# Kernel optimization log

Hardware: AMD Instinct MI355X
Metric: run time of the kernel (lower is better)

## Reference

```python
import jax, jax.numpy as jnp
import numpy as np

B, S, H = 1, 4096, 2048
NH, NKV, HD = 16, 4, 128  # query heads, kv heads, head_dim
THETA = 1000000.0
NEG = -1e9


def setup_inputs() -> dict:
    key = jax.random.key(0)
    ks = jax.random.split(key, 5)
    hidden_states = jax.random.normal(ks[0], (B, S, H), jnp.float32) * 0.02
    Wq = jax.random.normal(ks[1], (H, NH * HD), jnp.float32) * 0.02
    Wk = jax.random.normal(ks[2], (H, NKV * HD), jnp.float32) * 0.02
    Wv = jax.random.normal(ks[3], (H, NKV * HD), jnp.float32) * 0.02
    Wo = jax.random.normal(ks[4], (H, H), jnp.float32) * 0.02
    # additive causal mask [B,1,S,S]
    causal = jnp.tril(jnp.ones((S, S), bool))
    attention_mask = jnp.where(causal, 0.0, NEG).astype(jnp.float32)[None, None]
    position_ids = jnp.arange(S, dtype=jnp.int32)[None]
    return dict(hidden_states=hidden_states, Wq=Wq, Wk=Wk, Wv=Wv, Wo=Wo,
                attention_mask=attention_mask, position_ids=position_ids)


def _rotate_half(x):
    return jnp.concatenate([-x[..., HD // 2:], x[..., :HD // 2]], axis=-1)


def reference(hidden_states, Wq, Wk, Wv, Wo, attention_mask, position_ids):
    # projections -> [B, heads, S, HD]
    q = (hidden_states @ Wq).reshape(B, S, NH, HD).transpose(0, 2, 1, 3)
    k = (hidden_states @ Wk).reshape(B, S, NKV, HD).transpose(0, 2, 1, 3)
    v = (hidden_states @ Wv).reshape(B, S, NKV, HD).transpose(0, 2, 1, 3)

    # RoPE (HF style: freqs duplicated across halves, rotate_half)
    inv_freq = 1.0 / (THETA ** (jnp.arange(0, HD, 2, dtype=jnp.float32) / HD))
    freqs = position_ids.astype(jnp.float32)[..., None] * inv_freq  # [B,S,HD/2]
    emb = jnp.concatenate([freqs, freqs], axis=-1)                  # [B,S,HD]
    cos = jnp.cos(emb)[:, None].astype(q.dtype)                     # [B,1,S,HD]
    sin = jnp.sin(emb)[:, None].astype(q.dtype)
    q = q * cos + _rotate_half(q) * sin
    k = k * cos + _rotate_half(k) * sin

    # GQA: repeat each kv head consecutively (matches torch repeat_kv)
    rep = NH // NKV
    k = jnp.repeat(k, rep, axis=1)
    v = jnp.repeat(v, rep, axis=1)

    scale = 1.0 / jnp.sqrt(jnp.float32(HD))
    scores = jnp.einsum('bhqd,bhkd->bhqk', q, k) * scale + attention_mask
    attn = jax.nn.softmax(scores.astype(jnp.float32), axis=-1).astype(q.dtype)
    out = jnp.einsum('bhqk,bhkd->bhqd', attn, v)  # [B,NH,S,HD]
    out = out.transpose(0, 2, 1, 3).reshape(B, S, H)
    return out @ Wo
```

## Files before the change

### kernel.cpp

```cpp
#include <hip/hip_runtime.h>
#include <stdint.h>

typedef uint16_t u16;
typedef __bf16  bf16x8 __attribute__((ext_vector_type(8)));
typedef float   f32x4  __attribute__((ext_vector_type(4)));
typedef float   f32x16 __attribute__((ext_vector_type(16)));
typedef uint16_t u16x8 __attribute__((ext_vector_type(8), may_alias));
typedef uint32_t u32x4 __attribute__((ext_vector_type(4)));

typedef const __attribute__((address_space(1))) void* gas_p;
typedef __attribute__((address_space(3))) void* las_p;

__device__ __forceinline__ void load_lds16(const void* g, void* l) {
    __builtin_amdgcn_global_load_lds((gas_p)g, (las_p)l, 16, 0, 0);
}

__device__ __forceinline__ u16 f2bf(float f) {
    uint32_t u = __builtin_bit_cast(uint32_t, f);
    u += 0x7FFFu + ((u >> 16) & 1u);
    return (u16)(u >> 16);
}
__device__ __forceinline__ float bf2f(u16 h) {
    uint32_t u = ((uint32_t)h) << 16;
    return __builtin_bit_cast(float, u);
}
__device__ __forceinline__ bf16x8 ld_frag(const u16* p) {
    u16x8 t = *(const u16x8*)p;
    return __builtin_bit_cast(bf16x8, t);
}
__device__ __forceinline__ uint32_t cvt_pk_bf16(float lo, float hi) {
    uint32_t r;
    asm("v_cvt_pk_bf16_f32 %0, %1, %2" : "=v"(r) : "v"(lo), "v"(hi));
    return r;
}
__device__ __forceinline__ void plane32_swap(uint32_t& a, uint32_t& b) {
    asm("v_permlane32_swap_b32 %0, %1" : "+v"(a), "+v"(b));
}

__global__ __launch_bounds__(256) void convert_hidden(const float* __restrict__ in,
                                                      u16* __restrict__ out, int n8) {
    int i = blockIdx.x * 256 + threadIdx.x;
    if (i >= n8) return;
    const float* p = in + (size_t)i * 8;
    u16x8 o;
#pragma unroll
    for (int j = 0; j < 8; j++) o[j] = f2bf(p[j]);
    *(u16x8*)(out + (size_t)i * 8) = o;
}

__global__ __launch_bounds__(256) void transpose_cvt(const float* __restrict__ in,
                                                     u16* __restrict__ out,
                                                     int R, int C) {
    __shared__ u16 tile[64][65];
    const int tx = threadIdx.x;
    const int bc = blockIdx.x * 64;
    const int br = blockIdx.y * 64;
#pragma unroll
    for (int i = 0; i < 16; i++) {
        int idx = tx + i * 256;
        int r = idx >> 6, c = idx & 63;
        tile[r][c] = f2bf(in[(size_t)(br + r) * C + bc + c]);
    }
    __syncthreads();
#pragma unroll
    for (int i = 0; i < 16; i++) {
        int idx = tx + i * 256;
        int r = idx >> 6, c = idx & 63;
        out[(size_t)(bc + r) * R + br + c] = tile[c][r];
    }
}

__global__ __launch_bounds__(256) void transpose_b16(const u16* __restrict__ in,
                                                     u16* __restrict__ out,
                                                     int R, int C, int ldin, int off) {
    __shared__ u16 tile[64][65];
    const int tx = threadIdx.x;
    const int bc = blockIdx.x * 64;
    const int br = blockIdx.y * 64;
#pragma unroll
    for (int i = 0; i < 16; i++) {
        int idx = tx + i * 256;
        int r = idx >> 6, c = idx & 63;
        tile[r][c] = in[(size_t)(br + r) * ldin + off + bc + c];
    }
    __syncthreads();
#pragma unroll
    for (int i = 0; i < 16; i++) {
        int idx = tx + i * 256;
        int r = idx >> 6, c = idx & 63;
        out[(size_t)(bc + r) * R + br + c] = tile[c][r];
    }
}

#define TM 128
#define TN 128
#define TK 32

__global__ __launch_bounds__(256) void gemm_qkv(const u16* __restrict__ A,
                                                const u16* __restrict__ WqT,
                                                const u16* __restrict__ WkvT,
                                                u16* __restrict__ Qb,
                                                u16* __restrict__ KVb) {
    __shared__ u16 As[TM * TK];
    __shared__ u16 Bs[TN * TK];
    const int K = 2048;
    const int tid  = threadIdx.x;
    const int wave = tid >> 6;
    const int lane = tid & 63;
    const int l15  = lane & 15;
    const int quad = lane >> 4;
    const int m0 = blockIdx.y * TM;
    const int n0 = blockIdx.x * TN;
    const u16* Bt;
    u16* C;
    int ldC, cbase;
    if (n0 < 2048) { Bt = WqT + (size_t)n0 * K;          C = Qb;  ldC = 2048; cbase = n0; }
    else           { Bt = WkvT + (size_t)(n0 - 2048) * K; C = KVb; ldC = 1024; cbase = n0 - 2048; }
    const int wm = (wave >> 1) * 64;
    const int wn = (wave & 1) * 64;

    f32x4 acc[4][4] = {};

    const int srow = tid >> 2;
    const int scol = (tid & 3) * 8;
    const u16* Ap0 = A  + (size_t)(m0 + srow) * K + scol;
    const u16* Ap1 = A  + (size_t)(m0 + 64 + srow) * K + scol;
    const u16* Bp0 = Bt + (size_t)srow * K + scol;
    const u16* Bp1 = Bt + (size_t)(64 + srow) * K + scol;
    u16* AsD0 = As + wave * 512;
    u16* AsD1 = As + 2048 + wave * 512;
    u16* BsD0 = Bs + wave * 512;
    u16* BsD1 = Bs + 2048 + wave * 512;

    for (int k0 = 0; k0 < K; k0 += TK) {
        load_lds16(Ap0 + k0, AsD0);
        load_lds16(Ap1 + k0, AsD1);
        load_lds16(Bp0 + k0, BsD0);
        load_lds16(Bp1 + k0, BsD1);
        __syncthreads();
        bf16x8 af[4], bfr[4];
#pragma unroll
        for (int i = 0; i < 4; i++)
            af[i] = ld_frag(&As[(wm + i * 16 + l15) * TK + quad * 8]);
#pragma unroll
        for (int j = 0; j < 4; j++)
            bfr[j] = ld_frag(&Bs[(wn + j * 16 + l15) * TK + quad * 8]);
#pragma unroll
        for (int i = 0; i < 4; i++)
#pragma unroll
            for (int j = 0; j < 4; j++)
                acc[i][j] = __builtin_amdgcn_mfma_f32_16x16x32_bf16(af[i], bfr[j], acc[i][j], 0, 0, 0);
        __syncthreads();
    }
#pragma unroll
    for (int i = 0; i < 4; i++)
#pragma unroll
        for (int j = 0; j < 4; j++)
#pragma unroll
            for (int r = 0; r < 4; r++) {
                int row = m0 + wm + i * 16 + quad * 4 + r;
                int col = cbase + wn + j * 16 + l15;
                C[(size_t)row * ldC + col] = f2bf(acc[i][j][r]);
            }
}

template <bool F32OUT>
__global__ __launch_bounds__(256) void gemm_bt(const u16* __restrict__ A,
                                               const u16* __restrict__ Bt,
                                               void* __restrict__ Cp,
                                               int M, int N, int K) {
    __shared__ u16 As[TM * TK];
    __shared__ u16 Bs[TN * TK];
    const int tid  = threadIdx.x;
    const int wave = tid >> 6;
    const int lane = tid & 63;
    const int l15  = lane & 15;
    const int quad = lane >> 4;
    const int m0 = blockIdx.y * TM;
    const int n0 = blockIdx.x * TN;
    const int wm = (wave >> 1) * 64;
    const int wn = (wave & 1) * 64;

    f32x4 acc[4][4] = {};

    const int srow = tid >> 2;
    const int scol = (tid & 3) * 8;
    const u16* Ap0 = A  + (size_t)(m0 + srow) * K + scol;
    const u16* Ap1 = A  + (size_t)(m0 + 64 + srow) * K + scol;
    const u16* Bp0 = Bt + (size_t)(n0 + srow) * K + scol;
    const u16* Bp1 = Bt + (size_t)(n0 + 64 + srow) * K + scol;
    u16* AsD0 = As + wave * 512;
    u16* AsD1 = As + 2048 + wave * 512;
    u16* BsD0 = Bs + wave * 512;
    u16* BsD1 = Bs + 2048 + wave * 512;

    for (int k0 = 0; k0 < K; k0 += TK) {
        load_lds16(Ap0 + k0, AsD0);
        load_lds16(Ap1 + k0, AsD1);
        load_lds16(Bp0 + k0, BsD0);
        load_lds16(Bp1 + k0, BsD1);
        __syncthreads();
        bf16x8 af[4], bfr[4];
#pragma unroll
        for (int i = 0; i < 4; i++)
            af[i] = ld_frag(&As[(wm + i * 16 + l15) * TK + quad * 8]);
#pragma unroll
        for (int j = 0; j < 4; j++)
            bfr[j] = ld_frag(&Bs[(wn + j * 16 + l15) * TK + quad * 8]);
#pragma unroll
        for (int i = 0; i < 4; i++)
#pragma unroll
            for (int j = 0; j < 4; j++)
                acc[i][j] = __builtin_amdgcn_mfma_f32_16x16x32_bf16(af[i], bfr[j], acc[i][j], 0, 0, 0);
        __syncthreads();
    }
#pragma unroll
    for (int i = 0; i < 4; i++)
#pragma unroll
        for (int j = 0; j < 4; j++)
#pragma unroll
            for (int r = 0; r < 4; r++) {
                int row = m0 + wm + i * 16 + quad * 4 + r;
                int col = n0 + wn + j * 16 + l15;
                if (F32OUT)
                    ((float*)Cp)[(size_t)row * N + col] = acc[i][j][r];
                else
                    ((u16*)Cp)[(size_t)row * N + col] = f2bf(acc[i][j][r]);
            }
}

__global__ __launch_bounds__(256) void rope_kernel(u16* __restrict__ Q,
                                                   u16* __restrict__ KV) {
    int g = blockIdx.x * 256 + threadIdx.x;
    int d = g & 63;
    int row = g >> 6;
    int s = row / 20;
    int hh = row - s * 20;
    u16* buf = (hh < 16) ? (Q + (size_t)s * 2048 + hh * 128)
                         : (KV + (size_t)s * 1024 + (hh - 16) * 128);
    float p = (float)s;
    float angle = p * exp2f((float)d * (-19.931568569324174f / 64.0f));
    float c = cosf(angle), sn = sinf(angle);
    float x0 = bf2f(buf[d]), x1 = bf2f(buf[d + 64]);
    buf[d]      = f2bf(x0 * c - x1 * sn);
    buf[d + 64] = f2bf(x1 * c + x0 * sn);
}

#define SCALE2 0.1275430214486847f

__global__ __launch_bounds__(256, 2) void flash_attn4(const u16* __restrict__ Q,
                                                      const u16* __restrict__ KVb,
                                                      const u16* __restrict__ VT,
                                                      u16* __restrict__ O) {
    __shared__ u16 Ks[2][8192];
    __shared__ u16 Vs[2][8192];
    __shared__ float Llds[4][32];
    const int tid  = threadIdx.x;
    const int wave = tid >> 6;
    const int lane = tid & 63;
    const int l31  = lane & 31;
    const int hi8  = lane >> 5;
    const int bx   = blockIdx.x;
    const int h    = blockIdx.y;
    const int kvh  = h >> 2;
    const int q_lo = bx * 64;
    const int q_hi = (63 - bx) * 64;
    const int nlo  = bx + 1;
    const int nkv  = 64 - bx;

    const int qrow = (l31 < 16) ? (q_lo + wave * 16 + l31)
                                : (q_hi + wave * 16 + (l31 - 16));

    bf16x8 qf[8];
    {
        const u16* qp = Q + (size_t)qrow * 2048 + h * 128 + hi8 * 8;
#pragma unroll
        for (int dk = 0; dk < 8; dk++) qf[dk] = ld_frag(qp + dk * 16);
    }

    const u16* srcK[4];
    const u16* srcV[4];
#pragma unroll
    for (int r = 0; r < 4; r++) {
        int p = r * 256 + tid;
        int kv = p >> 4;
        srcK[r] = KVb + (size_t)kv * 1024 + kvh * 128 + ((((p & 15) - kv) & 15) * 8);
        int d = p >> 3;
        srcV[r] = VT + (size_t)(kvh * 128 + d) * 4096 + ((((p & 7) - (d & 7)) & 7) * 8);
    }

    f32x16 acc[4] = {};
    float l_run = 0.f;

#pragma unroll
    for (int r = 0; r < 4; r++) {
        load_lds16(srcK[r], &Ks[0][r * 2048 + wave * 512]);
        load_lds16(srcV[r], &Vs[0][r * 2048 + wave * 512]);
    }
    asm volatile("s_waitcnt vmcnt(0)" ::: "memory");
    __syncthreads();

    for (int kvb = 0; kvb < nkv; kvb++) {
        const int cur = kvb & 1;
        if (kvb + 1 < nkv) {
            const int kvn = (kvb + 1) * 64;
#pragma unroll
            for (int r = 0; r < 4; r++) {
                load_lds16(srcK[r] + (size_t)kvn * 1024, &Ks[cur ^ 1][r * 2048 + wave * 512]);
                load_lds16(srcV[r] + kvn, &Vs[cur ^ 1][r * 2048 + wave * 512]);
            }
        }
        const u16* Kb = Ks[cur];
        const u16* Vb = Vs[cur];
        const int kv0 = kvb * 64;
        const int mmode = (kvb == nlo - 1 || kvb == nkv - 1) ? 1 : ((kvb >= nlo) ? 2 : 0);
        const bool lodead = (l31 < 16);

#pragma unroll
        for (int cc = 0; cc < 2; cc++) {
            f32x16 sv = {};
            const int krow = cc * 32 + l31;
#pragma unroll
            for (int dk = 0; dk < 8; dk++) {
                int slot = ((dk * 2 + hi8) + krow) & 15;
                bf16x8 kf = ld_frag(&Kb[krow * 128 + slot * 8]);
                sv = __builtin_amdgcn_mfma_f32_32x32x16_bf16(kf, qf[dk], sv, 0, 0, 0);
            }
            float p[16];
            float rs = 0.f;
            if (mmode == 0) {
#pragma unroll
                for (int r = 0; r < 16; r++) {
                    float pe = exp2f(sv[r] * SCALE2);
                    p[r] = pe; rs += pe;
                }
            } else if (mmode == 1) {
                const int kvbase = kv0 + cc * 32 + 4 * hi8;
#pragma unroll
                for (int r = 0; r < 16; r++) {
                    float pe = exp2f(sv[r] * SCALE2);
                    int kvv = kvbase + (r & 3) + 8 * (r >> 2);
                    if (kvv > qrow) pe = 0.f;
                    p[r] = pe; rs += pe;
                }
            } else {
#pragma unroll
                for (int r = 0; r < 16; r++) {
                    float pe = exp2f(sv[r] * SCALE2);
                    if (lodead) pe = 0.f;
                    p[r] = pe; rs += pe;
                }
            }
            l_run += rs;

            uint32_t w0a = cvt_pk_bf16(p[0], p[1]);
            uint32_t w1a = cvt_pk_bf16(p[2], p[3]);
            uint32_t w2a = cvt_pk_bf16(p[4], p[5]);
            uint32_t w3a = cvt_pk_bf16(p[6], p[7]);
            plane32_swap(w0a, w2a);
            plane32_swap(w1a, w3a);
            uint32_t w0b = cvt_pk_bf16(p[8],  p[9]);
            uint32_t w1b = cvt_pk_bf16(p[10], p[11]);
            uint32_t w2b = cvt_pk_bf16(p[12], p[13]);
            uint32_t w3b = cvt_pk_bf16(p[14], p[15]);
            plane32_swap(w0b, w2b);
            plane32_swap(w1b, w3b);
            u32x4 paw0 = {w0a, w1a, w2a, w3a};
            u32x4 paw1 = {w0b, w1b, w2b, w3b};
            bf16x8 pa0 = __builtin_bit_cast(bf16x8, paw0);
            bf16x8 pa1 = __builtin_bit_cast(bf16x8, paw1);

#pragma unroll
            for (int ks2 = 0; ks2 < 2; ks2++) {
                bf16x8 pa = ks2 ? pa1 : pa0;
#pragma unroll
                for (int nt = 0; nt < 4; nt++) {
                    int d = nt * 32 + l31;
                    int slot = ((cc * 4 + ks2 * 2 + hi8) + d) & 7;
                    bf16x8 vf = ld_frag(&Vb[d * 64 + slot * 8]);
                    acc[nt] = __builtin_amdgcn_mfma_f32_32x32x16_bf16(pa, vf, acc[nt], 0, 0, 0);
                }
            }
        }
        asm volatile("s_waitcnt vmcnt(0)" ::: "memory");
        __syncthreads();
    }

    float l_tot = l_run + __shfl_xor(l_run, 32);
    if (lane < 32) Llds[wave][l31] = l_tot;
    __syncthreads();
#pragma unroll
    for (int r = 0; r < 16; r++) {
        int cr = (r & 3) + 8 * (r >> 2) + 4 * hi8;
        float linv = 1.0f / Llds[wave][cr];
        int row = (cr < 16) ? (q_lo + wave * 16 + cr) : (q_hi + wave * 16 + (cr - 16));
        u16* op = O + (size_t)row * 2048 + h * 128 + l31;
#pragma unroll
        for (int nt = 0; nt < 4; nt++)
            op[nt * 32] = f2bf(acc[nt][r] * linv);
    }
}

extern "C" void kernel_launch(void* const* d_in, const int* in_sizes, int n_in,
                              void* d_out, int out_size, void* d_ws, size_t ws_size,
                              hipStream_t stream) {
    const float* hidden = (const float*)d_in[0];
    const float* Wq = (const float*)d_in[1];
    const float* Wk = (const float*)d_in[2];
    const float* Wv = (const float*)d_in[3];
    const float* Wo = (const float*)d_in[4];
    float* out = (float*)d_out;

    u16* ws   = (u16*)d_ws;
    u16* Hb   = ws;
    u16* Qb   = Hb   + 8388608;
    u16* KVb  = Qb   + 8388608;
    u16* WqT  = KVb  + 4194304;
    u16* WkvT = WqT  + 4194304;
    u16* VT   = WkvT + 2097152;

    convert_hidden<<<4096, 256, 0, stream>>>(hidden, Hb, 1048576);

    transpose_cvt<<<dim3(32, 32), 256, 0, stream>>>(Wq, WqT, 2048, 2048);
    transpose_cvt<<<dim3(8, 32), 256, 0, stream>>>(Wk, WkvT, 2048, 512);
    transpose_cvt<<<dim3(8, 32), 256, 0, stream>>>(Wv, WkvT + 1048576, 2048, 512);

    gemm_qkv<<<dim3(24, 32), 256, 0, stream>>>(Hb, WqT, WkvT, Qb, KVb);

    u16* WoT = WqT;
    transpose_cvt<<<dim3(32, 32), 256, 0, stream>>>(Wo, WoT, 2048, 2048);

    rope_kernel<<<dim3(20480), 256, 0, stream>>>(Qb, KVb);

    transpose_b16<<<dim3(8, 64), 256, 0, stream>>>(KVb, VT, 4096, 512, 1024, 512);

    u16* Ob = Hb;
    flash_attn4<<<dim3(32, 16), 256, 0, stream>>>(Qb, KVb, VT, Ob);

    gemm_bt<true><<<dim3(16, 32), 256, 0, stream>>>(Ob, WoT, out, 4096, 2048, 2048);
}
```

Baseline: 461.2 us.

## Process two 32-row query tiles per wave in flash attention, folding scale into RoPE

The attention kernel now gives each wave two full 32-row query tiles (one low, one mirrored high) instead of half-dead mixed tiles, so each K/V fragment loaded from LDS feeds two MFMAs and masked-out lanes no longer waste compute. The softmax scale is folded into the RoPE step for Q, which removes a multiply per score. The grid is halved to 16x16 blocks with launch bounds of 1 block per SM and roughly doubled register use. This risks lower occupancy and only 256 blocks to spread across the CUs.

```diff
diff --git a/kernel.cpp b/kernel.cpp
--- a/kernel.cpp
+++ b/kernel.cpp
@@ -10,6 +10,8 @@
 
 typedef const __attribute__((address_space(1))) void* gas_p;
 typedef __attribute__((address_space(3))) void* las_p;
+
+#define SCALE2 0.1275430214486847f
 
 __device__ __forceinline__ void load_lds16(const void* g, void* l) {
     __builtin_amdgcn_global_load_lds((gas_p)g, (las_p)l, 16, 0, 0);
@@ -240,21 +242,74 @@
                          : (KV + (size_t)s * 1024 + (hh - 16) * 128);
     float p = (float)s;
     float angle = p * exp2f((float)d * (-19.931568569324174f / 64.0f));
-    float c = cosf(angle), sn = sinf(angle);
+    float sc = (hh < 16) ? SCALE2 : 1.0f;
+    float c = cosf(angle) * sc, sn = sinf(angle) * sc;
     float x0 = bf2f(buf[d]), x1 = bf2f(buf[d + 64]);
     buf[d]      = f2bf(x0 * c - x1 * sn);
     buf[d + 64] = f2bf(x1 * c + x0 * sn);
 }
 
-#define SCALE2 0.1275430214486847f
-
-__global__ __launch_bounds__(256, 2) void flash_attn4(const u16* __restrict__ Q,
+
+#define SMAX(CC, SV, QG, PA, LACC, MSK)                                        \
+  do {                                                                         \
+    float p_[16]; float rs_ = 0.f;                                             \
+    const int qrow_ = (QG) + l31;                                              \
+    const int kvbs_ = kv0 + (CC) * 32 + 4 * hi8;                               \
+    _Pragma("unroll")                                                          \
+    for (int r = 0; r < 16; r++) {                                             \
+      float pe = exp2f((SV)[r]);                                               \
+      if (MSK) { int kvv = kvbs_ + (r & 3) + 8 * (r >> 2);                     \
+                 pe = (kvv <= qrow_) ? pe : 0.f; }                             \
+      p_[r] = pe; rs_ += pe;                                                   \
+    }                                                                          \
+    LACC += rs_;                                                               \
+    uint32_t w0 = cvt_pk_bf16(p_[0], p_[1]);                                   \
+    uint32_t w1 = cvt_pk_bf16(p_[2], p_[3]);                                   \
+    uint32_t w2 = cvt_pk_bf16(p_[4], p_[5]);                                   \
+    uint32_t w3 = cvt_pk_bf16(p_[6], p_[7]);                                   \
+    plane32_swap(w0, w2); plane32_swap(w1, w3);                                \
+    uint32_t w4 = cvt_pk_bf16(p_[8], p_[9]);                                   \
+    uint32_t w5 = cvt_pk_bf16(p_[10], p_[11]);                                 \
+    uint32_t w6 = cvt_pk_bf16(p_[12], p_[13]);                                 \
+    uint32_t w7 = cvt_pk_bf16(p_[14], p_[15]);                                 \
+    plane32_swap(w4, w6); plane32_swap(w5, w7);                                \
+    u32x4 a0_ = {w0, w1, w2, w3}, a1_ = {w4, w5, w6, w7};                      \
+    PA[0] = __builtin_bit_cast(bf16x8, a0_);                                   \
+    PA[1] = __builtin_bit_cast(bf16x8, a1_);                                   \
+  } while (0)
+
+#define QK_CHUNK(CC, DOA, DOB, MSK)                                            \
+  do {                                                                         \
+    const int krow_ = (CC) * 32 + l31;                                         \
+    f32x16 svA_ = {}, svB_ = {};                                               \
+    _Pragma("unroll")                                                          \
+    for (int dk = 0; dk < 8; dk++) {                                           \
+      bf16x8 kf = ld_frag(&Kb[krow_ * 128 + (((dk * 2 + hi8) + krow_) & 15) * 8]); \
+      if (DOA) svA_ = __builtin_amdgcn_mfma_f32_32x32x16_bf16(kf, qfA[dk], svA_, 0, 0, 0); \
+      if (DOB) svB_ = __builtin_amdgcn_mfma_f32_32x32x16_bf16(kf, qfB[dk], svB_, 0, 0, 0); \
+    }                                                                          \
+    bf16x8 paA_[2], paB_[2];                                                   \
+    if (DOA) SMAX((CC), svA_, qg0A, paA_, lrA, (MSK));                         \
+    if (DOB) SMAX((CC), svB_, qg0B, paB_, lrB, (MSK));                         \
+    _Pragma("unroll")                                                          \
+    for (int ks2 = 0; ks2 < 2; ks2++) {                                        \
+      _Pragma("unroll")                                                        \
+      for (int nt = 0; nt < 4; nt++) {                                         \
+        const int d_ = nt * 32 + l31;                                          \
+        bf16x8 vf = ld_frag(&Vb[d_ * 64 + ((((CC) * 4 + ks2 * 2 + hi8) + d_) & 7) * 8]); \
+        if (DOA) accA[nt] = __builtin_amdgcn_mfma_f32_32x32x16_bf16(paA_[ks2], vf, accA[nt], 0, 0, 0); \
+        if (DOB) accB[nt] = __builtin_amdgcn_mfma_f32_32x32x16_bf16(paB_[ks2], vf, accB[nt], 0, 0, 0); \
+      }                                                                        \
+    }                                                                          \
+  } while (0)
+
+__global__ __launch_bounds__(256, 1) void flash_attn5(const u16* __restrict__ Q,
                                                       const u16* __restrict__ KVb,
                                                       const u16* __restrict__ VT,
                                                       u16* __restrict__ O) {
     __shared__ u16 Ks[2][8192];
     __shared__ u16 Vs[2][8192];
-    __shared__ float Llds[4][32];
+    __shared__ float Llds[4][2][32];
     const int tid  = threadIdx.x;
     const int wave = tid >> 6;
     const int lane = tid & 63;
@@ -263,19 +318,21 @@
     const int bx   = blockIdx.x;
     const int h    = blockIdx.y;
     const int kvh  = h >> 2;
-    const int q_lo = bx * 64;
-    const int q_hi = (63 - bx) * 64;
-    const int nlo  = bx + 1;
-    const int nkv  = 64 - bx;
-
-    const int qrow = (l31 < 16) ? (q_lo + wave * 16 + l31)
-                                : (q_hi + wave * 16 + (l31 - 16));
-
-    bf16x8 qf[8];
+    const int qg0A = bx * 128 + wave * 32;
+    const int qg0B = 3968 - bx * 128 + wave * 32;
+    const int dA   = qg0A >> 6;
+    const int dB   = qg0B >> 6;
+    const int nkv  = 64 - 2 * bx;
+
+    bf16x8 qfA[8], qfB[8];
     {
-        const u16* qp = Q + (size_t)qrow * 2048 + h * 128 + hi8 * 8;
-#pragma unroll
-        for (int dk = 0; dk < 8; dk++) qf[dk] = ld_frag(qp + dk * 16);
+        const u16* pa = Q + (size_t)(qg0A + l31) * 2048 + h * 128 + hi8 * 8;
+        const u16* pb = Q + (size_t)(qg0B + l31) * 2048 + h * 128 + hi8 * 8;
+#pragma unroll
+        for (int dk = 0; dk < 8; dk++) {
+            qfA[dk] = ld_frag(pa + dk * 16);
+            qfB[dk] = ld_frag(pb + dk * 16);
+        }
     }
 
     const u16* srcK[4];
@@ -289,8 +346,8 @@
         srcV[r] = VT + (size_t)(kvh * 128 + d) * 4096 + ((((p & 7) - (d & 7)) & 7) * 8);
     }
 
-    f32x16 acc[4] = {};
-    float l_run = 0.f;
+    f32x16 accA[4] = {}, accB[4] = {};
+    float lrA = 0.f, lrB = 0.f;
 
 #pragma unroll
     for (int r = 0; r < 4; r++) {
@@ -313,91 +370,41 @@
         const u16* Kb = Ks[cur];
         const u16* Vb = Vs[cur];
         const int kv0 = kvb * 64;
-        const int mmode = (kvb == nlo - 1 || kvb == nkv - 1) ? 1 : ((kvb >= nlo) ? 2 : 0);
-        const bool lodead = (l31 < 16);
-
-#pragma unroll
-        for (int cc = 0; cc < 2; cc++) {
-            f32x16 sv = {};
-            const int krow = cc * 32 + l31;
-#pragma unroll
-            for (int dk = 0; dk < 8; dk++) {
-                int slot = ((dk * 2 + hi8) + krow) & 15;
-                bf16x8 kf = ld_frag(&Kb[krow * 128 + slot * 8]);
-                sv = __builtin_amdgcn_mfma_f32_32x32x16_bf16(kf, qf[dk], sv, 0, 0, 0);
-            }
-            float p[16];
-            float rs = 0.f;
-            if (mmode == 0) {
-#pragma unroll
-                for (int r = 0; r < 16; r++) {
-                    float pe = exp2f(sv[r] * SCALE2);
-                    p[r] = pe; rs += pe;
-                }
-            } else if (mmode == 1) {
-                const int kvbase = kv0 + cc * 32 + 4 * hi8;
-#pragma unroll
-                for (int r = 0; r < 16; r++) {
-                    float pe = exp2f(sv[r] * SCALE2);
-                    int kvv = kvbase + (r & 3) + 8 * (r >> 2);
-                    if (kvv > qrow) pe = 0.f;
-                    p[r] = pe; rs += pe;
-                }
-            } else {
-#pragma unroll
-                for (int r = 0; r < 16; r++) {
-                    float pe = exp2f(sv[r] * SCALE2);
-                    if (lodead) pe = 0.f;
-                    p[r] = pe; rs += pe;
-                }
-            }
-            l_run += rs;
-
-            uint32_t w0a = cvt_pk_bf16(p[0], p[1]);
-            uint32_t w1a = cvt_pk_bf16(p[2], p[3]);
-            uint32_t w2a = cvt_pk_bf16(p[4], p[5]);
-            uint32_t w3a = cvt_pk_bf16(p[6], p[7]);
-            plane32_swap(w0a, w2a);
-            plane32_swap(w1a, w3a);
-            uint32_t w0b = cvt_pk_bf16(p[8],  p[9]);
-            uint32_t w1b = cvt_pk_bf16(p[10], p[11]);
-            uint32_t w2b = cvt_pk_bf16(p[12], p[13]);
-            uint32_t w3b = cvt_pk_bf16(p[14], p[15]);
-            plane32_swap(w0b, w2b);
-            plane32_swap(w1b, w3b);
-            u32x4 paw0 = {w0a, w1a, w2a, w3a};
-            u32x4 paw1 = {w0b, w1b, w2b, w3b};
-            bf16x8 pa0 = __builtin_bit_cast(bf16x8, paw0);
-            bf16x8 pa1 = __builtin_bit_cast(bf16x8, paw1);
-
-#pragma unroll
-            for (int ks2 = 0; ks2 < 2; ks2++) {
-                bf16x8 pa = ks2 ? pa1 : pa0;
-#pragma unroll
-                for (int nt = 0; nt < 4; nt++) {
-                    int d = nt * 32 + l31;
-                    int slot = ((cc * 4 + ks2 * 2 + hi8) + d) & 7;
-                    bf16x8 vf = ld_frag(&Vb[d * 64 + slot * 8]);
-                    acc[nt] = __builtin_amdgcn_mfma_f32_32x32x16_bf16(pa, vf, acc[nt], 0, 0, 0);
-                }
-            }
+
+        if (kvb == dA || kvb == dB) {
+            QK_CHUNK(0, 1, 1, 1);
+            QK_CHUNK(1, 1, 1, 1);
+        } else if (kvb < dA) {
+            QK_CHUNK(0, 1, 1, 0);
+            QK_CHUNK(1, 1, 1, 0);
+        } else if (kvb < dB) {
+            QK_CHUNK(0, 0, 1, 0);
+            QK_CHUNK(1, 0, 1, 0);
         }
+
         asm volatile("s_waitcnt vmcnt(0)" ::: "memory");
         __syncthreads();
     }
 
-    float l_tot = l_run + __shfl_xor(l_run, 32);
-    if (lane < 32) Llds[wave][l31] = l_tot;
+    float ltA = lrA + __shfl_xor(lrA, 32);
+    float ltB = lrB + __shfl_xor(lrB, 32);
+    if (lane < 32) {
+        Llds[wave][0][l31] = ltA;
+        Llds[wave][1][l31] = ltB;
+    }
     __syncthreads();
 #pragma unroll
     for (int r = 0; r < 16; r++) {
-        int cr = (r & 3) + 8 * (r >> 2) + 4 * hi8;
-        float linv = 1.0f / Llds[wave][cr];
-        int row = (cr < 16) ? (q_lo + wave * 16 + cr) : (q_hi + wave * 16 + (cr - 16));
-        u16* op = O + (size_t)row * 2048 + h * 128 + l31;
-#pragma unroll
-        for (int nt = 0; nt < 4; nt++)
-            op[nt * 32] = f2bf(acc[nt][r] * linv);
+        int qr = (r & 3) + 8 * (r >> 2) + 4 * hi8;
+        float liA = 1.0f / Llds[wave][0][qr];
+        float liB = 1.0f / Llds[wave][1][qr];
+        u16* opA = O + (size_t)(qg0A + qr) * 2048 + h * 128 + l31;
+        u16* opB = O + (size_t)(qg0B + qr) * 2048 + h * 128 + l31;
+#pragma unroll
+        for (int nt = 0; nt < 4; nt++) {
+            opA[nt * 32] = f2bf(accA[nt][r] * liA);
+            opB[nt * 32] = f2bf(accB[nt][r] * liB);
+        }
     }
 }
 
@@ -435,7 +442,7 @@
     transpose_b16<<<dim3(8, 64), 256, 0, stream>>>(KVb, VT, 4096, 512, 1024, 512);
 
     u16* Ob = Hb;
-    flash_attn4<<<dim3(32, 16), 256, 0, stream>>>(Qb, KVb, VT, Ob);
+    flash_attn5<<<dim3(16, 16), 256, 0, stream>>>(Qb, KVb, VT, Ob);
 
     gemm_bt<true><<<dim3(16, 32), 256, 0, stream>>>(Ob, WoT, out, 4096, 2048, 2048);
 }
```

After: 435.0 us. 1.06x faster.
